# Performance work log

Measured on AMD Instinct MI355X. Metric: run time of the kernel, lower is better.

## Reference

```python
import jax, jax.numpy as jnp
import numpy as np
import math

N = 8192
D_IN = 1024
D_H = 1024

def setup_inputs() -> dict:
    key = jax.random.key(0)
    k_h, k_q, k_k, k_v = jax.random.split(key, 4)
    s = 1.0 / math.sqrt(D_IN)
    return {
        "h": jax.random.normal(k_h, (N, D_IN), dtype=jnp.float32),
        "wq": jax.random.uniform(k_q, (D_H, D_IN), dtype=jnp.float32, minval=-s, maxval=s),
        "wk": jax.random.uniform(k_k, (D_H, D_IN), dtype=jnp.float32, minval=-s, maxval=s),
        "wv": jax.random.uniform(k_v, (D_H, D_IN), dtype=jnp.float32, minval=-s, maxval=s),
    }

def reference(h, wq, wk, wv):
    # nn.Linear with no bias: x @ W.T
    q = h @ wq.T  # [N, D_H]
    k = h @ wk.T  # [N, D_H]
    v = h @ wv.T  # [N, D_H]
    scale = 1.0 / math.sqrt(q.shape[-1])
    z = (q @ k.T) * scale          # [N, N]
    beta = jax.nn.softmax(z, axis=1)
    return beta @ v                 # [N, D_H]
```

## Files before the change

### kernel.cpp

```cpp
#include <hip/hip_runtime.h>
#include <hip/hip_bf16.h>
#include <stdint.h>
#include <math.h>

typedef __bf16 bf16;
typedef __bf16 bf16x8 __attribute__((ext_vector_type(8)));
typedef __bf16 bf16x4 __attribute__((ext_vector_type(4)));
typedef float  f32x4  __attribute__((ext_vector_type(4)));
typedef int    i32x4  __attribute__((ext_vector_type(4)));

#define AS_GLOBAL __attribute__((address_space(1)))
#define AS_LDS    __attribute__((address_space(3)))

__device__ __forceinline__ void gload_lds16(const void* g, void* l) {
    __builtin_amdgcn_global_load_lds((const AS_GLOBAL uint32_t*)g,
                                     (AS_LDS uint32_t*)l, 16, 0, 0);
}
__device__ __forceinline__ void cfence() { asm volatile("" ::: "memory"); }
#define BAR()    do { cfence(); __builtin_amdgcn_s_barrier(); cfence(); } while (0)
#define WAITV(n) asm volatile("s_waitcnt vmcnt(" #n ")" ::: "memory")
#define WAITL0() asm volatile("s_waitcnt lgkmcnt(0)" ::: "memory")

#define QSC 36.0f
#define QDQ (1.0f / (QSC * QSC * 32.0f))

__device__ __forceinline__ int qi8(float f) {
    int q = (int)rintf(f);
    return q > 127 ? 127 : (q < -127 ? -127 : q);
}

__global__ __launch_bounds__(256) void cvt_f32_to_bf16(const float* __restrict__ in,
                                                       bf16* __restrict__ out, int n4) {
    int i = blockIdx.x * 256 + threadIdx.x;
    if (i >= n4) return;
    const float4* p = (const float4*)in;
    float4 v = p[i];
    bf16x4 o;
    o[0] = (bf16)v.x; o[1] = (bf16)v.y; o[2] = (bf16)v.z; o[3] = (bf16)v.w;
    *(bf16x4*)(out + (size_t)i * 4) = o;
}

__global__ __launch_bounds__(256) void zero_f32(float* __restrict__ p, int n) {
    int i = blockIdx.x * 256 + threadIdx.x;
    if (i < n) p[i] = 0.f;
}

template<typename CT, int BN, int SPLIT, int EPI>
__global__ __launch_bounds__(512, 2) void gemmW(const bf16* __restrict__ A,
                                                const bf16* __restrict__ B,
                                                CT* __restrict__ C,
                                                CT* __restrict__ C2,
                                                int8_t* __restrict__ q8,
                                                int8_t* __restrict__ k8,
                                                bf16* __restrict__ vb,
                                                int K, int lda, int ldb, int ldc,
                                                int nbn) {
    constexpr int NBH = BN / 128;
    constexpr int NR  = BN / 64;
    constexpr int NHF = NR / 2;
    __shared__ char smem[65536 + NBH * 32768];

    const int tid  = threadIdx.x;
    const int lane = tid & 63;
    const int wave = tid >> 6;
    const int wr   = wave >> 2;
    const int wc   = wave & 3;
    const int frow = lane & 15;
    const int fg   = lane >> 4;

    const int cpx = gridDim.x >> 3;
    const int swz = ((int)blockIdx.x & 7) * cpx + ((int)blockIdx.x >> 3);
    int id = swz, s = 0;
    if (SPLIT == 2) { s = id & 1; id >>= 1; }
    const int bm = id / nbn, bn = id % nbn;
    const int NT = K >> 6;
    const size_t koff = (size_t)s * K;
    CT* Cp = (SPLIT == 2 && s == 1) ? C2 : C;

    const int r0 = tid >> 3;
    const int c0 = ((tid & 7) ^ (r0 & 7)) << 3;
    const bf16* Abase = A + (size_t)(bm * 256 + r0) * lda + c0 + koff;
    const bf16* Bbase = B + (size_t)(bn * BN + r0) * ldb + c0 + koff;

    auto stA = [&](int t, int h) {
        char* d = smem + ((t & 1) << 15) + (h << 14) + (tid << 4);
        gload_lds16(Abase + ((size_t)(h * 128)      ) * lda + t * 64, d);
        gload_lds16(Abase + ((size_t)(h * 128) + 64 ) * lda + t * 64, d + 8192);
    };
    auto stB = [&](int t, int h) {
        char* d = smem + 65536 + (t & 1) * (NBH * 16384) + (h << 14) + (tid << 4);
        gload_lds16(Bbase + ((size_t)(h * 128)      ) * ldb + t * 64, d);
        gload_lds16(Bbase + ((size_t)(h * 128) + 64 ) * ldb + t * 64, d + 8192);
    };
    auto rdA = [&](int t, int m, int kk) -> bf16x8 {
        int r = m * 16 + frow;
        return *(const bf16x8*)(smem + ((t & 1) << 15) + (wr << 14)
                + r * 128 + ((((kk << 2) + fg) ^ (frow & 7)) << 4));
    };
    auto rdB = [&](int t, int n, int kk) -> bf16x8 {
        int br = wc * (BN / 4) + n * 16 + frow;
        return *(const bf16x8*)(smem + 65536 + (t & 1) * (NBH * 16384) + ((br >> 7) << 14)
                + (br & 127) * 128 + ((((kk << 2) + fg) ^ (frow & 7)) << 4));
    };

    f32x4 acc[8][NR] = {};
    bf16x8 aLo[4][2], aHi[4][2], bLo[NHF][2], bHi[NHF][2];

#define MMQ(MO, NO, AARR, BARR) \
    _Pragma("unroll") for (int m_ = 0; m_ < 4; ++m_) \
    _Pragma("unroll") for (int n_ = 0; n_ < NHF; ++n_) \
    _Pragma("unroll") for (int k_ = 0; k_ < 2; ++k_) \
        acc[m_ + MO][n_ + NO] = __builtin_amdgcn_mfma_f32_16x16x32_bf16( \
            AARR[m_][k_], BARR[n_][k_], acc[m_ + MO][n_ + NO], 0, 0, 0);

    stA(0, 0); stA(0, 1);
    stB(0, 0); if constexpr (NBH == 2) stB(0, 1);
    stA(1, 0); stA(1, 1);
    if constexpr (NBH == 2) { stB(1, 0); WAITV(6); } else { WAITV(4); }
    BAR();

    for (int t = 0; t < NT; ++t) {
        if (t + 1 < NT) stB(t + 1, NBH - 1);
        #pragma unroll
        for (int m_ = 0; m_ < 4; ++m_) { aLo[m_][0] = rdA(t, m_, 0); aLo[m_][1] = rdA(t, m_, 1); }
        #pragma unroll
        for (int n_ = 0; n_ < NHF; ++n_) { bLo[n_][0] = rdB(t, n_, 0); bLo[n_][1] = rdB(t, n_, 1); }
        #pragma unroll
        for (int n_ = 0; n_ < NHF; ++n_) { bHi[n_][0] = rdB(t, NHF + n_, 0); bHi[n_][1] = rdB(t, NHF + n_, 1); }
        #pragma unroll
        for (int m_ = 0; m_ < 4; ++m_) { aHi[m_][0] = rdA(t, 4 + m_, 0); aHi[m_][1] = rdA(t, 4 + m_, 1); }
        __builtin_amdgcn_s_setprio(1);
        MMQ(0, 0, aLo, bLo);
        MMQ(0, NHF, aLo, bHi);
        __builtin_amdgcn_s_setprio(0);
        WAITL0();
        BAR();
        if (t + 2 < NT) {
            stA(t + 2, 0); stA(t + 2, 1);
            if constexpr (NBH == 2) stB(t + 2, 0);
        }
        __builtin_amdgcn_s_setprio(1);
        MMQ(4, NHF, aHi, bHi);
        MMQ(4, 0, aHi, bLo);
        __builtin_amdgcn_s_setprio(0);
        if (t + 2 < NT) {
            if constexpr (NBH == 2) WAITV(6); else WAITV(4);
        } else if (t + 1 < NT) {
            WAITV(0);
        }
        BAR();
    }
#undef MMQ

    const size_t crow0 = (size_t)bm * 256 + wr * 128 + (fg << 2);
    const size_t ccol0 = (size_t)bn * BN + wc * (BN / 4) + frow;
    if constexpr (EPI == 1) {
        const int panel = (int)(ccol0 >> 10);
        const size_t pcol0 = ccol0 & 1023;
        #pragma unroll
        for (int m = 0; m < 8; ++m)
            #pragma unroll
            for (int n = 0; n < NR; ++n)
                #pragma unroll
                for (int i = 0; i < 4; ++i) {
                    float v = acc[m][n][i];
                    size_t row = crow0 + m * 16 + i;
                    size_t col = pcol0 + n * 16;
                    if (panel == 0)
                        q8[row * 1024 + col] = (int8_t)qi8(v * QSC);
                    else if (panel == 1)
                        k8[row * 1024 + col] = (int8_t)qi8(v * QSC);
                    else
                        vb[row * 1024 + col] = (bf16)v;
                }
    } else {
        #pragma unroll
        for (int m = 0; m < 8; ++m)
            #pragma unroll
            for (int n = 0; n < NR; ++n)
                #pragma unroll
                for (int i = 0; i < 4; ++i)
                    Cp[(crow0 + m * 16 + i) * ldc + ccol0 + n * 16] = (CT)(acc[m][n][i]);
    }
}

__global__ __launch_bounds__(512, 2) void gemmEi8(const int8_t* __restrict__ A,
                                                  const int8_t* __restrict__ B,
                                                  bf16* __restrict__ E,
                                                  float* __restrict__ sums,
                                                  int K, int ld, int ldc, int nbn) {
    __shared__ char smem[131072];

    const int tid  = threadIdx.x;
    const int lane = tid & 63;
    const int wave = tid >> 6;
    const int wr   = wave >> 2;
    const int wc   = wave & 3;
    const int frow = lane & 15;
    const int fg   = lane >> 4;

    const int cpx = gridDim.x >> 3;
    const int swz = ((int)blockIdx.x & 7) * cpx + ((int)blockIdx.x >> 3);
    const int bm = swz / nbn, bn = swz % nbn;
    const int NT = K >> 7;

    const int r0 = tid >> 3;
    const int c0 = ((tid & 7) ^ (r0 & 7)) << 4;
    const int8_t* Abase = A + (size_t)(bm * 256 + r0) * ld + c0;
    const int8_t* Bbase = B + (size_t)(bn * 256 + r0) * ld + c0;

    auto stA = [&](int t, int h) {
        char* d = smem + ((t & 1) << 15) + (h << 14) + (tid << 4);
        gload_lds16(Abase + ((size_t)(h * 128)     ) * ld + t * 128, d);
        gload_lds16(Abase + ((size_t)(h * 128) + 64) * ld + t * 128, d + 8192);
    };
    auto stB = [&](int t, int h) {
        char* d = smem + 65536 + ((t & 1) << 15) + (h << 14) + (tid << 4);
        gload_lds16(Bbase + ((size_t)(h * 128)     ) * ld + t * 128, d);
        gload_lds16(Bbase + ((size_t)(h * 128) + 64) * ld + t * 128, d + 8192);
    };
    auto rdA = [&](int t, int m, int kk) -> i32x4 {
        int r = m * 16 + frow;
        return *(const i32x4*)(smem + ((t & 1) << 15) + (wr << 14)
                + r * 128 + ((((kk << 2) + fg) ^ (frow & 7)) << 4));
    };
    auto rdB = [&](int t, int n, int kk) -> i32x4 {
        int br = wc * 64 + n * 16 + frow;
        return *(const i32x4*)(smem + 65536 + ((t & 1) << 15) + ((br >> 7) << 14)
                + (br & 127) * 128 + ((((kk << 2) + fg) ^ (frow & 7)) << 4));
    };

    i32x4 acc[8][4] = {};
    i32x4 aLo[4][2], aHi[4][2], bLo[2][2], bHi[2][2];

#define MMQ(MO, NO, AARR, BARR) \
    _Pragma("unroll") for (int m_ = 0; m_ < 4; ++m_) \
    _Pragma("unroll") for (int n_ = 0; n_ < 2; ++n_) \
    _Pragma("unroll") for (int k_ = 0; k_ < 2; ++k_) \
        acc[m_ + MO][n_ + NO] = __builtin_amdgcn_mfma_i32_16x16x64_i8( \
            AARR[m_][k_], BARR[n_][k_], acc[m_ + MO][n_ + NO], 0, 0, 0);

    stA(0, 0); stA(0, 1);
    stB(0, 0); stB(0, 1);
    stA(1, 0); stA(1, 1);
    stB(1, 0); WAITV(6);
    BAR();

    for (int t = 0; t < NT; ++t) {
        if (t + 1 < NT) stB(t + 1, 1);
        #pragma unroll
        for (int m_ = 0; m_ < 4; ++m_) { aLo[m_][0] = rdA(t, m_, 0); aLo[m_][1] = rdA(t, m_, 1); }
        #pragma unroll
        for (int n_ = 0; n_ < 2; ++n_) { bLo[n_][0] = rdB(t, n_, 0); bLo[n_][1] = rdB(t, n_, 1); }
        #pragma unroll
        for (int n_ = 0; n_ < 2; ++n_) { bHi[n_][0] = rdB(t, 2 + n_, 0); bHi[n_][1] = rdB(t, 2 + n_, 1); }
        #pragma unroll
        for (int m_ = 0; m_ < 4; ++m_) { aHi[m_][0] = rdA(t, 4 + m_, 0); aHi[m_][1] = rdA(t, 4 + m_, 1); }
        __builtin_amdgcn_s_setprio(1);
        MMQ(0, 0, aLo, bLo);
        MMQ(0, 2, aLo, bHi);
        __builtin_amdgcn_s_setprio(0);
        WAITL0();
        BAR();
        if (t + 2 < NT) { stA(t + 2, 0); stA(t + 2, 1); stB(t + 2, 0); }
        __builtin_amdgcn_s_setprio(1);
        MMQ(4, 2, aHi, bHi);
        MMQ(4, 0, aHi, bLo);
        __builtin_amdgcn_s_setprio(0);
        if (t + 2 < NT)      { WAITV(6); }
        else if (t + 1 < NT) { WAITV(0); }
        BAR();
    }
#undef MMQ

    const size_t crow0 = (size_t)bm * 256 + wr * 128 + (fg << 2);
    const size_t ccol0 = (size_t)bn * 256 + wc * 64 + frow;
    float* part = (float*)smem;
    const int rl0 = wr * 128 + (fg << 2);
    const int ent = wc * 16 + frow;
    #pragma unroll
    for (int m = 0; m < 8; ++m)
        #pragma unroll
        for (int i = 0; i < 4; ++i) {
            float s = 0.f;
            #pragma unroll
            for (int n = 0; n < 4; ++n) {
                float e = __expf((float)acc[m][n][i] * QDQ);
                bf16 b = (bf16)e;
                E[(crow0 + m * 16 + i) * ldc + ccol0 + n * 16] = b;
                s += (float)b;
            }
            part[(rl0 + m * 16 + i) * 66 + ent] = s;
        }
    __syncthreads();
    if (tid < 256) {
        float s = 0.f;
        const float* pr = part + tid * 66;
        #pragma unroll 8
        for (int e = 0; e < 64; ++e) s += pr[e];
        atomicAdd(&sums[(size_t)bm * 256 + tid], s);
    }
}

__global__ __launch_bounds__(256) void add_scale(float* __restrict__ out,
                                                 const float* __restrict__ part,
                                                 const float* __restrict__ sums, int n4) {
    int i = blockIdx.x * 256 + threadIdx.x;
    if (i >= n4) return;
    const float sc = 1.0f / sums[i >> 8];
    float4 a = ((const float4*)out)[i];
    float4 b = ((const float4*)part)[i];
    a.x = (a.x + b.x) * sc; a.y = (a.y + b.y) * sc;
    a.z = (a.z + b.z) * sc; a.w = (a.w + b.w) * sc;
    ((float4*)out)[i] = a;
}

__global__ __launch_bounds__(256) void transpose_bf16(const ushort* __restrict__ V,
                                                      ushort* __restrict__ VT,
                                                      int R, int ld) {
    __shared__ ushort tile[32][33];
    const int tx = threadIdx.x, ty = threadIdx.y;
    const int r0 = blockIdx.y * 32, c0 = blockIdx.x * 32;
    #pragma unroll
    for (int i = 0; i < 32; i += 8)
        tile[ty + i][tx] = V[(size_t)(r0 + ty + i) * ld + c0 + tx];
    __syncthreads();
    #pragma unroll
    for (int i = 0; i < 32; i += 8)
        VT[(size_t)(c0 + ty + i) * R + r0 + tx] = tile[tx][ty + i];
}

extern "C" void kernel_launch(void* const* d_in, const int* in_sizes, int n_in,
                              void* d_out, int out_size, void* d_ws, size_t ws_size,
                              hipStream_t stream) {
    const float* h  = (const float*)d_in[0];
    const float* wq = (const float*)d_in[1];
    const float* wk = (const float*)d_in[2];
    const float* wv = (const float*)d_in[3];
    float* out = (float*)d_out;

    char* ws = (char*)d_ws;
    bf16*   h_bf = (bf16*)(ws);
    bf16*   wcat = (bf16*)(ws + (16ull << 20));
    int8_t* Qi8  = (int8_t*)(ws + (22ull << 20));
    int8_t* Ki8  = (int8_t*)(ws + (30ull << 20));
    bf16*   Vb   = (bf16*)(ws + (38ull << 20));
    bf16*   VT   = (bf16*)(ws + (54ull << 20));
    bf16*   E    = (bf16*)(ws + (70ull << 20));
    float*  Pv   = (float*)(ws);
    float*  sums = (float*)(ws + (198ull << 20));

    cvt_f32_to_bf16<<<8192, 256, 0, stream>>>(h,  h_bf, (8192 * 1024) / 4);
    cvt_f32_to_bf16<<<1024, 256, 0, stream>>>(wq, wcat,               (1024 * 1024) / 4);
    cvt_f32_to_bf16<<<1024, 256, 0, stream>>>(wk, wcat + 1024 * 1024, (1024 * 1024) / 4);
    cvt_f32_to_bf16<<<1024, 256, 0, stream>>>(wv, wcat + 2048 * 1024, (1024 * 1024) / 4);
    zero_f32<<<32, 256, 0, stream>>>(sums, 8192);

    gemmW<bf16, 256, 1, 1><<<384, 512, 0, stream>>>(h_bf, wcat, nullptr, nullptr,
                                                    Qi8, Ki8, Vb,
                                                    1024, 1024, 1024, 1024, 12);

    transpose_bf16<<<dim3(32, 256), dim3(32, 8), 0, stream>>>(
        (const ushort*)Vb, (ushort*)VT, 8192, 1024);

    gemmEi8<<<1024, 512, 0, stream>>>(Qi8, Ki8, E, sums, 1024, 1024, 8192, 32);

    gemmW<float, 256, 2, 0><<<256, 512, 0, stream>>>(E, VT, out, Pv,
                                                     nullptr, nullptr, nullptr,
                                                     4096, 8192, 8192, 1024, 4);

    add_scale<<<8192, 256, 0, stream>>>(out, Pv, sums, (8192 * 1024) / 4);
}
```

Measured before the change: 327.0 us.

## Fuse V transpose into projection epilogue and softmax normalization into PV GEMM

The projection GEMM now writes V already transposed through an LDS staging tile, which removes the separate transpose kernel and the intermediate V buffer. The split-K PV GEMM now scales its accumulators by 1/rowsum and atomically adds them into a pre-zeroed output. This drops the partial buffer and the add_scale pass. In exchange it adds a full-output zeroing kernel and many float atomics in the epilogue, and the split-K summation order becomes nondeterministic.

After: 332.8 us. About the same (+1.8%).

```diff
diff --git a/kernel.cpp b/kernel.cpp
--- a/kernel.cpp
+++ b/kernel.cpp
@@ -40,9 +40,9 @@
     *(bf16x4*)(out + (size_t)i * 4) = o;
 }
 
-__global__ __launch_bounds__(256) void zero_f32(float* __restrict__ p, int n) {
+__global__ __launch_bounds__(256) void zero_f32v4(float* __restrict__ p, int n4) {
     int i = blockIdx.x * 256 + threadIdx.x;
-    if (i < n) p[i] = 0.f;
+    if (i < n4) ((float4*)p)[i] = make_float4(0.f, 0.f, 0.f, 0.f);
 }
 
 template<typename CT, int BN, int SPLIT, int EPI>
@@ -52,7 +52,8 @@
                                                 CT* __restrict__ C2,
                                                 int8_t* __restrict__ q8,
                                                 int8_t* __restrict__ k8,
-                                                bf16* __restrict__ vb,
+                                                bf16* __restrict__ vt,
+                                                const float* __restrict__ sums,
                                                 int K, int lda, int ldb, int ldc,
                                                 int nbn) {
     constexpr int NBH = BN / 128;
@@ -157,22 +158,58 @@
     if constexpr (EPI == 1) {
         const int panel = (int)(ccol0 >> 10);
         const size_t pcol0 = ccol0 & 1023;
+        if (panel < 2) {
+            int8_t* dst = (panel == 0) ? q8 : k8;
+            #pragma unroll
+            for (int m = 0; m < 8; ++m)
+                #pragma unroll
+                for (int n = 0; n < NR; ++n)
+                    #pragma unroll
+                    for (int i = 0; i < 4; ++i)
+                        dst[(crow0 + m * 16 + i) * 1024 + pcol0 + n * 16] =
+                            (int8_t)qi8(acc[m][n][i] * QSC);
+        } else {
+            bf16* tl = (bf16*)smem;
+            const int vcb  = (bn & 3) * 256;
+            const int lrow = wr * 128 + (fg << 2);
+            #pragma unroll
+            for (int h = 0; h < 2; ++h) {
+                BAR();
+                if ((wc >> 1) == h) {
+                    const int lc = (wc & 1) * 64 + frow;
+                    #pragma unroll
+                    for (int m = 0; m < 8; ++m)
+                        #pragma unroll
+                        for (int n = 0; n < 4; ++n) {
+                            bf16x4 v;
+                            #pragma unroll
+                            for (int i = 0; i < 4; ++i) v[i] = (bf16)acc[m][n][i];
+                            *(bf16x4*)&tl[(lc + n * 16) * 264 + lrow + m * 16] = v;
+                        }
+                }
+                BAR();
+                #pragma unroll
+                for (int j = 0; j < 8; ++j) {
+                    int cid = j * 512 + tid;
+                    int c   = cid >> 5;
+                    int rc  = (cid & 31) << 3;
+                    bf16x8 v = *(const bf16x8*)&tl[c * 264 + rc];
+                    *(bf16x8*)&vt[(size_t)(vcb + h * 128 + c) * 8192 + bm * 256 + rc] = v;
+                }
+            }
+        }
+    } else if constexpr (EPI == 2) {
         #pragma unroll
         for (int m = 0; m < 8; ++m)
             #pragma unroll
-            for (int n = 0; n < NR; ++n)
+            for (int i = 0; i < 4; ++i) {
+                const size_t row = crow0 + m * 16 + i;
+                const float inv = 1.0f / sums[row];
                 #pragma unroll
-                for (int i = 0; i < 4; ++i) {
-                    float v = acc[m][n][i];
-                    size_t row = crow0 + m * 16 + i;
-                    size_t col = pcol0 + n * 16;
-                    if (panel == 0)
-                        q8[row * 1024 + col] = (int8_t)qi8(v * QSC);
-                    else if (panel == 1)
-                        k8[row * 1024 + col] = (int8_t)qi8(v * QSC);
-                    else
-                        vb[row * 1024 + col] = (bf16)v;
-                }
+                for (int n = 0; n < NR; ++n)
+                    atomicAdd((float*)&C[row * ldc + ccol0 + n * 16],
+                              acc[m][n][i] * inv);
+            }
     } else {
         #pragma unroll
         for (int m = 0; m < 8; ++m)
@@ -302,34 +339,6 @@
     }
 }
 
-__global__ __launch_bounds__(256) void add_scale(float* __restrict__ out,
-                                                 const float* __restrict__ part,
-                                                 const float* __restrict__ sums, int n4) {
-    int i = blockIdx.x * 256 + threadIdx.x;
-    if (i >= n4) return;
-    const float sc = 1.0f / sums[i >> 8];
-    float4 a = ((const float4*)out)[i];
-    float4 b = ((const float4*)part)[i];
-    a.x = (a.x + b.x) * sc; a.y = (a.y + b.y) * sc;
-    a.z = (a.z + b.z) * sc; a.w = (a.w + b.w) * sc;
-    ((float4*)out)[i] = a;
-}
-
-__global__ __launch_bounds__(256) void transpose_bf16(const ushort* __restrict__ V,
-                                                      ushort* __restrict__ VT,
-                                                      int R, int ld) {
-    __shared__ ushort tile[32][33];
-    const int tx = threadIdx.x, ty = threadIdx.y;
-    const int r0 = blockIdx.y * 32, c0 = blockIdx.x * 32;
-    #pragma unroll
-    for (int i = 0; i < 32; i += 8)
-        tile[ty + i][tx] = V[(size_t)(r0 + ty + i) * ld + c0 + tx];
-    __syncthreads();
-    #pragma unroll
-    for (int i = 0; i < 32; i += 8)
-        VT[(size_t)(c0 + ty + i) * R + r0 + tx] = tile[tx][ty + i];
-}
-
 extern "C" void kernel_launch(void* const* d_in, const int* in_sizes, int n_in,
                               void* d_out, int out_size, void* d_ws, size_t ws_size,
                               hipStream_t stream) {
@@ -344,30 +353,24 @@
     bf16*   wcat = (bf16*)(ws + (16ull << 20));
     int8_t* Qi8  = (int8_t*)(ws + (22ull << 20));
     int8_t* Ki8  = (int8_t*)(ws + (30ull << 20));
-    bf16*   Vb   = (bf16*)(ws + (38ull << 20));
-    bf16*   VT   = (bf16*)(ws + (54ull << 20));
-    bf16*   E    = (bf16*)(ws + (70ull << 20));
-    float*  Pv   = (float*)(ws);
-    float*  sums = (float*)(ws + (198ull << 20));
+    bf16*   VT   = (bf16*)(ws + (38ull << 20));
+    bf16*   E    = (bf16*)(ws + (54ull << 20));
+    float*  sums = (float*)(ws + (182ull << 20));
 
     cvt_f32_to_bf16<<<8192, 256, 0, stream>>>(h,  h_bf, (8192 * 1024) / 4);
     cvt_f32_to_bf16<<<1024, 256, 0, stream>>>(wq, wcat,               (1024 * 1024) / 4);
     cvt_f32_to_bf16<<<1024, 256, 0, stream>>>(wk, wcat + 1024 * 1024, (1024 * 1024) / 4);
     cvt_f32_to_bf16<<<1024, 256, 0, stream>>>(wv, wcat + 2048 * 1024, (1024 * 1024) / 4);
-    zero_f32<<<32, 256, 0, stream>>>(sums, 8192);
+    zero_f32v4<<<8, 256, 0, stream>>>(sums, 8192 / 4);
+    zero_f32v4<<<8192, 256, 0, stream>>>(out, (8192 * 1024) / 4);
 
     gemmW<bf16, 256, 1, 1><<<384, 512, 0, stream>>>(h_bf, wcat, nullptr, nullptr,
-                                                    Qi8, Ki8, Vb,
+                                                    Qi8, Ki8, VT, nullptr,
                                                     1024, 1024, 1024, 1024, 12);
 
-    transpose_bf16<<<dim3(32, 256), dim3(32, 8), 0, stream>>>(
-        (const ushort*)Vb, (ushort*)VT, 8192, 1024);
-
     gemmEi8<<<1024, 512, 0, stream>>>(Qi8, Ki8, E, sums, 1024, 1024, 8192, 32);
 
-    gemmW<float, 256, 2, 0><<<256, 512, 0, stream>>>(E, VT, out, Pv,
-                                                     nullptr, nullptr, nullptr,
+    gemmW<float, 256, 2, 2><<<256, 512, 0, stream>>>(E, VT, out, nullptr,
+                                                     nullptr, nullptr, nullptr, sums,
                                                      4096, 8192, 8192, 1024, 4);
-
-    add_scale<<<8192, 256, 0, stream>>>(out, Pv, sums, (8192 * 1024) / 4);
-}
+}
```
